# Performance work log

Measured on AMD Instinct MI355X. Metric: run time of the kernel, lower is better.

The kernel has to match this reference:

```python
import jax, jax.numpy as jnp
import numpy as np

NUM_HEADS = 8
FOCUSING_FACTOR = 3.0
EPS = 1e-6


def setup_inputs() -> dict:
    key = jax.random.key(0)
    ks = jax.random.split(key, 5)
    B, C, H, W = 16, 256, 64, 64
    hd = C // NUM_HEADS
    return {
        "x": jax.random.normal(ks[0], (B, C, H, W), jnp.float32),
        "qkv_w": jax.random.normal(ks[1], (3 * C, C), jnp.float32) * 0.02,
        "qkv_b": jnp.zeros((3 * C,), jnp.float32),
        "proj_w": jax.random.normal(ks[2], (C, C), jnp.float32) * 0.02,
        "proj_b": jnp.zeros((C,), jnp.float32),
        "dwc_w": jax.random.normal(ks[3], (hd, 1, 5, 5), jnp.float32) * 0.02,
        "dwc_b": jnp.zeros((hd,), jnp.float32),
        "scale": jnp.zeros((1, 1, C), jnp.float32),
    }


def reference(x, qkv_w, qkv_b, proj_w, proj_b, dwc_w, dwc_b, scale):
    B, C, H, W = x.shape
    N = H * W
    hd = C // NUM_HEADS

    # b c h w -> b (h w) c
    xf = x.reshape(B, C, N).transpose(0, 2, 1)
    qkv = xf @ qkv_w.T + qkv_b  # [B, N, 3C]
    q, k, v = jnp.split(qkv, 3, axis=-1)

    # focusing feature map
    q = jax.nn.relu(q) + EPS
    k = jax.nn.relu(k) + EPS
    sc = jax.nn.softplus(scale)
    q = q / sc
    k = k / sc
    q_norm = jnp.linalg.norm(q, axis=-1, keepdims=True)
    k_norm = jnp.linalg.norm(k, axis=-1, keepdims=True)
    # focusing_factor <= 6 branch
    q = q ** FOCUSING_FACTOR
    k = k ** FOCUSING_FACTOR
    q = q / jnp.linalg.norm(q, axis=-1, keepdims=True) * q_norm
    k = k / jnp.linalg.norm(k, axis=-1, keepdims=True) * k_norm

    # b n (h c) -> (b h) n c
    def to_heads(t):
        return t.reshape(B, N, NUM_HEADS, hd).transpose(0, 2, 1, 3).reshape(B * NUM_HEADS, N, hd)

    q, k, v = to_heads(q), to_heads(k), to_heads(v)

    i, j, c, d = N, N, hd, hd
    z = 1.0 / (jnp.einsum('bic,bc->bi', q, k.sum(axis=1)) + EPS)
    if i * j * (c + d) > c * d * (i + j):
        kv = jnp.einsum('bjc,bjd->bcd', k, v)  # [(BH), c, d]
        out = jnp.einsum('bic,bcd,bi->bid', q, kv, z)
    else:
        qk = jnp.einsum('bic,bjc->bij', q, k)
        out = jnp.einsum('bij,bjd,bi->bid', qk, v, z)

    # depthwise conv on v: b (w h) c -> b c w h (square map)
    num = int(N ** 0.5)
    fm = v.transpose(0, 2, 1).reshape(B * NUM_HEADS, hd, num, num)
    fm = jax.lax.conv_general_dilated(
        fm, dwc_w, window_strides=(1, 1), padding='SAME',
        feature_group_count=hd,
        dimension_numbers=('NCHW', 'OIHW', 'NCHW')) + dwc_b[None, :, None, None]
    fm = fm.reshape(B * NUM_HEADS, hd, N).transpose(0, 2, 1)
    out = out + fm

    # (b h) n c -> b n (h c)
    out = out.reshape(B, NUM_HEADS, N, hd).transpose(0, 2, 1, 3).reshape(B, N, C)
    out = out @ proj_w.T + proj_b
    # b (h w) c -> b c h w
    return out.transpose(0, 2, 1).reshape(B, C, H, W)
```

## Files before the change

### kernel.cpp

```cpp
#include <hip/hip_runtime.h>
#include <cmath>

#define B_   16
#define C_   256
#define HW_  64
#define N_   4096
#define NH_  8
#define HD_  32
#define M_   (B_ * N_)
#define QKVC (3 * C_)
#define EPS_ 1e-6f

typedef short bf16x8 __attribute__((ext_vector_type(8)));
typedef float f32x4 __attribute__((ext_vector_type(4)));
typedef unsigned int u32x4 __attribute__((ext_vector_type(4)));

__device__ __forceinline__ float b2f(unsigned short u) {
  union { unsigned int i; float f; } v;
  v.i = ((unsigned int)u) << 16;
  return v.f;
}
__device__ __forceinline__ float blo(unsigned int u) {
  union { unsigned int i; float f; } v; v.i = u << 16; return v.f;
}
__device__ __forceinline__ float bhi(unsigned int u) {
  union { unsigned int i; float f; } v; v.i = u & 0xffff0000u; return v.f;
}
__device__ __forceinline__ unsigned short f2b(float f) {
  union { float f; unsigned int i; } v;
  v.f = f;
  unsigned int r = v.i + 0x7FFFu + ((v.i >> 16) & 1u);
  return (unsigned short)(r >> 16);
}
__device__ __forceinline__ void gload_lds16(const void* g, void* l) {
  __builtin_amdgcn_global_load_lds(
      (const __attribute__((address_space(1))) void*)g,
      (__attribute__((address_space(3))) void*)l, 16, 0, 0);
}

__global__ __launch_bounds__(256) void k_cast_x(const float* __restrict__ x,
                                                unsigned short* __restrict__ xT) {
  __shared__ float t[32][33];
  const int n0 = blockIdx.x * 32, c0 = blockIdx.y * 32, b = blockIdx.z;
  const int tid = threadIdx.x;
  const int r = tid >> 3, g = (tid & 7) * 4;
  float4 v = *reinterpret_cast<const float4*>(
      &x[((size_t)(b * C_ + c0 + r)) * N_ + n0 + g]);
  t[r][g + 0] = v.x; t[r][g + 1] = v.y; t[r][g + 2] = v.z; t[r][g + 3] = v.w;
  __syncthreads();
  ushort4 o;
  o.x = f2b(t[g + 0][r]); o.y = f2b(t[g + 1][r]);
  o.z = f2b(t[g + 2][r]); o.w = f2b(t[g + 3][r]);
  *reinterpret_cast<ushort4*>(&xT[((size_t)(b * N_ + n0 + r)) * C_ + c0 + g]) = o;
}

__global__ __launch_bounds__(256) void k_cast_w(const float* __restrict__ w1,
                                                const float* __restrict__ w2,
                                                unsigned short* __restrict__ dst) {
  const int g4 = (blockIdx.x * 256 + threadIdx.x) * 4;
  float4 v;
  if (g4 < 196608) v = *reinterpret_cast<const float4*>(w1 + g4);
  else             v = *reinterpret_cast<const float4*>(w2 + (g4 - 196608));
  ushort4 o;
  o.x = f2b(v.x); o.y = f2b(v.y); o.z = f2b(v.z); o.w = f2b(v.w);
  *reinterpret_cast<ushort4*>(dst + g4) = o;
}

__global__ void k_prep_scale(const float* __restrict__ scale,
                             float* __restrict__ rsc) {
  const int c = threadIdx.x;
  rsc[c] = 1.f / log1pf(expf(scale[c]));
}

template <int LDA, int OUTMODE, int NCOL>
__global__ __launch_bounds__(256) void k_gemm(
    const unsigned short* __restrict__ A, const unsigned short* __restrict__ W,
    const float* __restrict__ bias, void* __restrict__ outp) {
  __shared__ unsigned short As[128 * 64];
  __shared__ unsigned short Bs[128 * 64];
  const int tid = threadIdx.x;
  const int wid = tid >> 6, lane = tid & 63;
  const int lin = blockIdx.x + blockIdx.y * 512;
  const int bandp = lin >> 3;
  const int rowb = bandp / NCOL;
  const int colb = bandp - rowb * NCOL;
  const int m0 = (((lin & 7) << 6) + rowb) * 128;
  const int col0 = colb * 128;
  const int wr = wid >> 1, wc = wid & 1;

  const int lrow = lane >> 3;
  const int sl = (lane & 7) ^ (lrow & 7);

  f32x4 acc[4][4];
#pragma unroll
  for (int i = 0; i < 4; ++i)
#pragma unroll
    for (int j = 0; j < 4; ++j) acc[i][j] = (f32x4){0.f, 0.f, 0.f, 0.f};

  for (int kt = 0; kt < 4; ++kt) {
    const int k0 = kt * 64;
#pragma unroll
    for (int q = 0; q < 4; ++q) {
      const int chunk = wid * 4 + q;
      const int row = chunk * 8 + lrow;
      gload_lds16(A + (size_t)(m0 + row) * LDA + k0 + sl * 8, &As[chunk * 512]);
      gload_lds16(W + (size_t)(col0 + row) * 256 + k0 + sl * 8, &Bs[chunk * 512]);
    }
    __syncthreads();

    bf16x8 fa[2][4], fb[2][4];
#pragma unroll
    for (int i = 0; i < 4; ++i) {
      const int ra = wr * 64 + i * 16 + (lane & 15);
      const int rb = wc * 64 + i * 16 + (lane & 15);
#pragma unroll
      for (int ks = 0; ks < 2; ++ks) {
        const int s = ks * 4 + (lane >> 4);
        fa[ks][i] = *reinterpret_cast<const bf16x8*>(
            &As[ra * 64 + ((s ^ (ra & 7)) * 8)]);
        fb[ks][i] = *reinterpret_cast<const bf16x8*>(
            &Bs[rb * 64 + ((s ^ (rb & 7)) * 8)]);
      }
    }
#pragma unroll
    for (int i = 0; i < 4; ++i)
#pragma unroll
      for (int j = 0; j < 4; ++j) {
        acc[i][j] = __builtin_amdgcn_mfma_f32_16x16x32_bf16(fa[0][i], fb[0][j],
                                                            acc[i][j], 0, 0, 0);
        acc[i][j] = __builtin_amdgcn_mfma_f32_16x16x32_bf16(fa[1][i], fb[1][j],
                                                            acc[i][j], 0, 0, 0);
      }
    __syncthreads();
  }

  if (OUTMODE == 0) {
    unsigned short* O = (unsigned short*)outp;
#pragma unroll
    for (int j = 0; j < 4; ++j) {
      const int colg = col0 + wc * 64 + j * 16 + (lane & 15);
      const float bb = bias[colg];
#pragma unroll
      for (int i = 0; i < 4; ++i) {
        const int mrow = m0 + wr * 64 + i * 16 + ((lane >> 4) << 2);
#pragma unroll
        for (int r = 0; r < 4; ++r)
          O[(size_t)(mrow + r) * QKVC + colg] = f2b(acc[i][j][r] + bb);
      }
    }
  } else {
    float* O = (float*)outp;
    const int b = m0 >> 12;
    const int nb0 = (m0 & 4095) + wr * 64;
#pragma unroll
    for (int j = 0; j < 4; ++j) {
      const int colg = col0 + wc * 64 + j * 16 + (lane & 15);
      const float bb = bias[colg];
#pragma unroll
      for (int i = 0; i < 4; ++i) {
        const int nb = nb0 + i * 16 + ((lane >> 4) << 2);
        f32x4 o = acc[i][j];
        o += bb;
        __builtin_nontemporal_store(
            o, reinterpret_cast<f32x4*>(&O[((size_t)(b * C_ + colg)) * N_ + nb]));
      }
    }
  }
}

__global__ __launch_bounds__(256) void k_focus(unsigned short* __restrict__ qkv,
                                               const float* __restrict__ rsc) {
  const int wave = threadIdx.x >> 6, lane = threadIdx.x & 63;
  const int t = blockIdx.x * 4 + wave;
  const size_t base = (size_t)t * QKVC + lane * 4;

  uint2 qu = *reinterpret_cast<const uint2*>(qkv + base);
  uint2 ku = *reinterpret_cast<const uint2*>(qkv + base + C_);
  const f32x4 rs = *reinterpret_cast<const f32x4*>(rsc + lane * 4);

  float q[4], k[4], q3[4], k3[4];
  q[0] = blo(qu.x); q[1] = bhi(qu.x); q[2] = blo(qu.y); q[3] = bhi(qu.y);
  k[0] = blo(ku.x); k[1] = bhi(ku.x); k[2] = blo(ku.y); k[3] = bhi(ku.y);

  float sq2 = 0.f, sq6 = 0.f, sk2 = 0.f, sk6 = 0.f;
#pragma unroll
  for (int i = 0; i < 4; ++i) {
    q[i] = (fmaxf(q[i], 0.f) + EPS_) * rs[i];
    k[i] = (fmaxf(k[i], 0.f) + EPS_) * rs[i];
    const float q2 = q[i] * q[i], k2 = k[i] * k[i];
    q3[i] = q2 * q[i];
    k3[i] = k2 * k[i];
    sq2 += q2; sk2 += k2;
    sq6 += q3[i] * q3[i];
    sk6 += k3[i] * k3[i];
  }
#pragma unroll
  for (int off = 1; off < 64; off <<= 1) {
    sq2 += __shfl_xor(sq2, off);
    sq6 += __shfl_xor(sq6, off);
    sk2 += __shfl_xor(sk2, off);
    sk6 += __shfl_xor(sk6, off);
  }
  const float fq = sqrtf(sq2 / sq6);
  const float fk = sqrtf(sk2 / sk6);

  uint2 oq, ok;
  oq.x = (unsigned int)f2b(q3[0] * fq) | ((unsigned int)f2b(q3[1] * fq) << 16);
  oq.y = (unsigned int)f2b(q3[2] * fq) | ((unsigned int)f2b(q3[3] * fq) << 16);
  ok.x = (unsigned int)f2b(k3[0] * fk) | ((unsigned int)f2b(k3[1] * fk) << 16);
  ok.y = (unsigned int)f2b(k3[2] * fk) | ((unsigned int)f2b(k3[3] * fk) << 16);
  *reinterpret_cast<uint2*>(qkv + base) = oq;
  *reinterpret_cast<uint2*>(qkv + base + C_) = ok;
}

#define KVP_CHUNKS 16
__global__ __launch_bounds__(256) void k_kv_part(
    const unsigned short* __restrict__ qkv, float* __restrict__ kvp,
    float* __restrict__ ksp) {
  const int bh = blockIdx.x;
  const int chunk = blockIdx.y;
  const int b = bh >> 3, h = bh & 7;
  const int tid = threadIdx.x;
  __shared__ float ksf[64 * 36];
  __shared__ float vsf[64 * 36];

  const int c = tid >> 3;
  const int d0 = (tid & 7) * 4;
  const int srow = tid >> 2;
  const int sseg = (tid & 3) * 8;
  const int j0 = chunk * 256;

  float a0 = 0.f, a1 = 0.f, a2 = 0.f, a3 = 0.f, ksum = 0.f;

  uint4 ku, vu;
  {
    const size_t rb = ((size_t)(b * N_ + j0 + srow)) * QKVC + h * HD_ + sseg;
    ku = *reinterpret_cast<const uint4*>(qkv + rb + C_);
    vu = *reinterpret_cast<const uint4*>(qkv + rb + 2 * C_);
  }

  for (int t = 0; t < 4; ++t) {
    {
      f32x4 k0 = {blo(ku.x), bhi(ku.x), blo(ku.y), bhi(ku.y)};
      f32x4 k1 = {blo(ku.z), bhi(ku.z), blo(ku.w), bhi(ku.w)};
      f32x4 v0 = {blo(vu.x), bhi(vu.x), blo(vu.y), bhi(vu.y)};
      f32x4 v1 = {blo(vu.z), bhi(vu.z), blo(vu.w), bhi(vu.w)};
      *reinterpret_cast<f32x4*>(&ksf[srow * 36 + sseg]) = k0;
      *reinterpret_cast<f32x4*>(&ksf[srow * 36 + sseg + 4]) = k1;
      *reinterpret_cast<f32x4*>(&vsf[srow * 36 + sseg]) = v0;
      *reinterpret_cast<f32x4*>(&vsf[srow * 36 + sseg + 4]) = v1;
    }
    __syncthreads();
    if (t < 3) {
      const size_t rb =
          ((size_t)(b * N_ + j0 + (t + 1) * 64 + srow)) * QKVC + h * HD_ + sseg;
      ku = *reinterpret_cast<const uint4*>(qkv + rb + C_);
      vu = *reinterpret_cast<const uint4*>(qkv + rb + 2 * C_);
    }
#pragma unroll 8
    for (int jj = 0; jj < 64; ++jj) {
      const float kc = ksf[jj * 36 + c];
      const f32x4 vv = *reinterpret_cast<const f32x4*>(&vsf[jj * 36 + d0]);
      a0 += kc * vv[0];
      a1 += kc * vv[1];
      a2 += kc * vv[2];
      a3 += kc * vv[3];
      ksum += kc;
    }
    __syncthreads();
  }

  float* kvo = kvp + ((size_t)chunk * 128 + bh) * 1024 + c * 32 + d0;
  kvo[0] = a0; kvo[1] = a1; kvo[2] = a2; kvo[3] = a3;
  if ((tid & 7) == 0) ksp[((size_t)chunk * 128 + bh) * 32 + c] = ksum;
}

__global__ __launch_bounds__(256) void k_attn_mfma(
    unsigned short* __restrict__ qkv, const float* __restrict__ kvp,
    const float* __restrict__ ksp) {
  const int bh = blockIdx.y;
  const int b = bh >> 3, h = bh & 7;
  const int tid = threadIdx.x;
  const int lane = tid & 63;
  const int r0 = blockIdx.x * 256 + (tid >> 6) * 64;

  __shared__ float kv_s[1024];
  __shared__ float ksum_s[32];
  for (int pp = tid; pp < 1024; pp += 256) {
    float s = 0.f;
#pragma unroll
    for (int ch = 0; ch < KVP_CHUNKS; ++ch)
      s += kvp[((size_t)ch * 128 + bh) * 1024 + pp];
    kv_s[pp] = s;
  }
  if (tid < 32) {
    float s = 0.f;
#pragma unroll
    for (int ch = 0; ch < KVP_CHUNKS; ++ch)
      s += ksp[((size_t)ch * 128 + bh) * 32 + tid];
    ksum_s[tid] = s;
  }
  __syncthreads();

  const int kb = (lane >> 4) * 8;
  const int col = lane & 15;
  bf16x8 bhi0, bhi1, blo0, blo1;
  float ks0[8];
#pragma unroll
  for (int t = 0; t < 8; ++t) {
    const float v0 = kv_s[(kb + t) * 32 + col];
    const float v1 = kv_s[(kb + t) * 32 + col + 16];
    const unsigned short h0 = f2b(v0), h1 = f2b(v1);
    ((unsigned short*)&bhi0)[t] = h0;
    ((unsigned short*)&bhi1)[t] = h1;
    ((unsigned short*)&blo0)[t] = f2b(v0 - b2f(h0));
    ((unsigned short*)&blo1)[t] = f2b(v1 - b2f(h1));
    ks0[t] = ksum_s[kb + t];
  }

#pragma unroll
  for (int rt = 0; rt < 4; ++rt) {
    const int row = r0 + rt * 16 + (lane & 15);
    const bf16x8 a = *reinterpret_cast<const bf16x8*>(
        qkv + (size_t)(b * N_ + row) * QKVC + h * HD_ + kb);
    float zp = 0.f;
#pragma unroll
    for (int t = 0; t < 8; ++t) zp += b2f(((const unsigned short*)&a)[t]) * ks0[t];
    zp += __shfl_xor(zp, 16);
    zp += __shfl_xor(zp, 32);
    const float z = 1.f / (zp + EPS_);

    f32x4 acc0 = {0.f, 0.f, 0.f, 0.f}, acc1 = {0.f, 0.f, 0.f, 0.f};
    acc0 = __builtin_amdgcn_mfma_f32_16x16x32_bf16(a, blo0, acc0, 0, 0, 0);
    acc1 = __builtin_amdgcn_mfma_f32_16x16x32_bf16(a, blo1, acc1, 0, 0, 0);
    acc0 = __builtin_amdgcn_mfma_f32_16x16x32_bf16(a, bhi0, acc0, 0, 0, 0);
    acc1 = __builtin_amdgcn_mfma_f32_16x16x32_bf16(a, bhi1, acc1, 0, 0, 0);

#pragma unroll
    for (int r = 0; r < 4; ++r) {
      const int rr = (lane >> 4) * 4 + r;
      const float zr = __shfl(z, rr);
      unsigned short* op =
          qkv + (size_t)(b * N_ + r0 + rt * 16 + rr) * QKVC + h * HD_;
      op[col] = f2b(acc0[r] * zr);
      op[col + 16] = f2b(acc1[r] * zr);
    }
  }
}

__global__ __launch_bounds__(256) void k_conv(
    unsigned short* __restrict__ qkv, const float* __restrict__ dwc_w,
    const float* __restrict__ dwc_b) {
  const int lin = blockIdx.x;
  const int g2 = (lin & 7) * 256 + (lin >> 3);
  const int bh = g2 >> 4;
  const int ig = g2 & 15;
  const int i0 = ig * 4;
  const int b = bh >> 3, h = bh & 7;
  const int tid = threadIdx.x;
  const int j = tid >> 2;
  const int g = tid & 3;
  const int d0 = g * 8;
  const int wave = tid >> 6, lane = tid & 63;

  __shared__ float w_s[800];
  __shared__ float b_s[32];
  __shared__ unsigned short v_s[8 * 64 * 32];

#pragma unroll
  for (int rr = 0; rr < 8; ++rr) {
    const int ii = i0 + rr - 2;
    if (ii < 0 || ii >= 64) continue;
    gload_lds16(qkv + ((size_t)(b * N_ + ii * 64 + wave * 16 + (lane >> 2))) * QKVC +
                    2 * C_ + h * HD_ + (lane & 3) * 8,
                &v_s[rr * 2048 + wave * 512]);
  }
  for (int p = tid; p < 800; p += 256)
    w_s[p] = dwc_w[(p & 31) * 25 + (p >> 5)];
  if (tid < 32) b_s[tid] = dwc_b[tid];
  __syncthreads();

#pragma unroll
  for (int r = 0; r < 4; ++r) {
    const int i = i0 + r;
    float fm[8];
#pragma unroll
    for (int dd = 0; dd < 8; ++dd) fm[dd] = b_s[d0 + dd];
#pragma unroll
    for (int kr = 0; kr < 5; ++kr) {
      const int ii = i + kr - 2;
      if (ii < 0 || ii >= 64) continue;
      const int lr = r + kr;
#pragma unroll
      for (int kj = 0; kj < 5; ++kj) {
        const int jj = j + kj - 2;
        if (jj < 0 || jj >= 64) continue;
        const unsigned int* vr = reinterpret_cast<const unsigned int*>(
            &v_s[lr * 2048 + jj * 32 + d0]);
        const float* wt = &w_s[(kr * 5 + kj) * 32 + d0];
#pragma unroll
        for (int p = 0; p < 4; ++p) {
          const unsigned int vu = vr[p];
          fm[2 * p + 0] += blo(vu) * wt[2 * p + 0];
          fm[2 * p + 1] += bhi(vu) * wt[2 * p + 1];
        }
      }
    }
    unsigned int* orow = reinterpret_cast<unsigned int*>(
        qkv + ((size_t)(b * N_ + i * 64 + j)) * QKVC + h * HD_ + d0);
    uint4 cur = *reinterpret_cast<const uint4*>(orow);
    unsigned int o[4] = {cur.x, cur.y, cur.z, cur.w};
#pragma unroll
    for (int p = 0; p < 4; ++p) {
      const unsigned int lo = f2b(blo(o[p]) + fm[2 * p + 0]);
      const unsigned int hi = f2b(bhi(o[p]) + fm[2 * p + 1]);
      o[p] = lo | (hi << 16);
    }
    *reinterpret_cast<uint4*>(orow) = make_uint4(o[0], o[1], o[2], o[3]);
  }
}

extern "C" void kernel_launch(void* const* d_in, const int* in_sizes, int n_in,
                              void* d_out, int out_size, void* d_ws,
                              size_t ws_size, hipStream_t stream) {
  (void)in_sizes; (void)n_in; (void)out_size; (void)ws_size;
  const float* x      = (const float*)d_in[0];
  const float* qkv_w  = (const float*)d_in[1];
  const float* qkv_b  = (const float*)d_in[2];
  const float* proj_w = (const float*)d_in[3];
  const float* proj_b = (const float*)d_in[4];
  const float* dwc_w  = (const float*)d_in[5];
  const float* dwc_b  = (const float*)d_in[6];
  const float* scale  = (const float*)d_in[7];
  float* out = (float*)d_out;

  char* w = (char*)d_ws;
  unsigned short* xT   = (unsigned short*)w; w += (size_t)M_ * C_ * 2;
  unsigned short* qkvb = (unsigned short*)w; w += (size_t)M_ * QKVC * 2;
  unsigned short* wq   = (unsigned short*)w; w += (size_t)(QKVC + C_) * C_ * 2;
  unsigned short* wp   = wq + (size_t)QKVC * C_;
  float* kvp   = (float*)w;                  w += (size_t)KVP_CHUNKS * 128 * 1024 * 4;
  float* ksp   = (float*)w;                  w += (size_t)KVP_CHUNKS * 128 * 32 * 4;
  float* rscb  = (float*)w;                  w += 256 * 4;

  k_prep_scale<<<1, 256, 0, stream>>>(scale, rscb);
  k_cast_x<<<dim3(N_ / 32, C_ / 32, B_), 256, 0, stream>>>(x, xT);
  k_cast_w<<<256, 256, 0, stream>>>(qkv_w, proj_w, wq);
  k_gemm<256, 0, 6><<<dim3(512, 6), 256, 0, stream>>>(
      xT, wq, qkv_b, (void*)qkvb);
  k_focus<<<M_ / 4, 256, 0, stream>>>(qkvb, rscb);
  k_kv_part<<<dim3(128, KVP_CHUNKS), 256, 0, stream>>>(qkvb, kvp, ksp);
  k_attn_mfma<<<dim3(N_ / 256, 128), 256, 0, stream>>>(qkvb, kvp, ksp);
  k_conv<<<2048, 256, 0, stream>>>(qkvb, dwc_w, dwc_b);
  k_gemm<768, 1, 2><<<dim3(512, 2), 256, 0, stream>>>(
      qkvb, wp, proj_b, (void*)out);
}
```

Baseline: 210.7 us.

## Fuse attention output and depthwise conv into one kernel; drop nontemporal stores

Measured after the change: 202.8 us. -3.8%, faster.

```diff
diff --git a/kernel.cpp b/kernel.cpp
--- a/kernel.cpp
+++ b/kernel.cpp
@@ -161,8 +161,7 @@
         const int nb = nb0 + i * 16 + ((lane >> 4) << 2);
         f32x4 o = acc[i][j];
         o += bb;
-        __builtin_nontemporal_store(
-            o, reinterpret_cast<f32x4*>(&O[((size_t)(b * C_ + colg)) * N_ + nb]));
+        *reinterpret_cast<f32x4*>(&O[((size_t)(b * C_ + colg)) * N_ + nb]) = o;
       }
     }
   }
@@ -275,81 +274,9 @@
   if ((tid & 7) == 0) ksp[((size_t)chunk * 128 + bh) * 32 + c] = ksum;
 }
 
-__global__ __launch_bounds__(256) void k_attn_mfma(
+__global__ __launch_bounds__(256) void k_attn_conv_f(
     unsigned short* __restrict__ qkv, const float* __restrict__ kvp,
-    const float* __restrict__ ksp) {
-  const int bh = blockIdx.y;
-  const int b = bh >> 3, h = bh & 7;
-  const int tid = threadIdx.x;
-  const int lane = tid & 63;
-  const int r0 = blockIdx.x * 256 + (tid >> 6) * 64;
-
-  __shared__ float kv_s[1024];
-  __shared__ float ksum_s[32];
-  for (int pp = tid; pp < 1024; pp += 256) {
-    float s = 0.f;
-#pragma unroll
-    for (int ch = 0; ch < KVP_CHUNKS; ++ch)
-      s += kvp[((size_t)ch * 128 + bh) * 1024 + pp];
-    kv_s[pp] = s;
-  }
-  if (tid < 32) {
-    float s = 0.f;
-#pragma unroll
-    for (int ch = 0; ch < KVP_CHUNKS; ++ch)
-      s += ksp[((size_t)ch * 128 + bh) * 32 + tid];
-    ksum_s[tid] = s;
-  }
-  __syncthreads();
-
-  const int kb = (lane >> 4) * 8;
-  const int col = lane & 15;
-  bf16x8 bhi0, bhi1, blo0, blo1;
-  float ks0[8];
-#pragma unroll
-  for (int t = 0; t < 8; ++t) {
-    const float v0 = kv_s[(kb + t) * 32 + col];
-    const float v1 = kv_s[(kb + t) * 32 + col + 16];
-    const unsigned short h0 = f2b(v0), h1 = f2b(v1);
-    ((unsigned short*)&bhi0)[t] = h0;
-    ((unsigned short*)&bhi1)[t] = h1;
-    ((unsigned short*)&blo0)[t] = f2b(v0 - b2f(h0));
-    ((unsigned short*)&blo1)[t] = f2b(v1 - b2f(h1));
-    ks0[t] = ksum_s[kb + t];
-  }
-
-#pragma unroll
-  for (int rt = 0; rt < 4; ++rt) {
-    const int row = r0 + rt * 16 + (lane & 15);
-    const bf16x8 a = *reinterpret_cast<const bf16x8*>(
-        qkv + (size_t)(b * N_ + row) * QKVC + h * HD_ + kb);
-    float zp = 0.f;
-#pragma unroll
-    for (int t = 0; t < 8; ++t) zp += b2f(((const unsigned short*)&a)[t]) * ks0[t];
-    zp += __shfl_xor(zp, 16);
-    zp += __shfl_xor(zp, 32);
-    const float z = 1.f / (zp + EPS_);
-
-    f32x4 acc0 = {0.f, 0.f, 0.f, 0.f}, acc1 = {0.f, 0.f, 0.f, 0.f};
-    acc0 = __builtin_amdgcn_mfma_f32_16x16x32_bf16(a, blo0, acc0, 0, 0, 0);
-    acc1 = __builtin_amdgcn_mfma_f32_16x16x32_bf16(a, blo1, acc1, 0, 0, 0);
-    acc0 = __builtin_amdgcn_mfma_f32_16x16x32_bf16(a, bhi0, acc0, 0, 0, 0);
-    acc1 = __builtin_amdgcn_mfma_f32_16x16x32_bf16(a, bhi1, acc1, 0, 0, 0);
-
-#pragma unroll
-    for (int r = 0; r < 4; ++r) {
-      const int rr = (lane >> 4) * 4 + r;
-      const float zr = __shfl(z, rr);
-      unsigned short* op =
-          qkv + (size_t)(b * N_ + r0 + rt * 16 + rr) * QKVC + h * HD_;
-      op[col] = f2b(acc0[r] * zr);
-      op[col + 16] = f2b(acc1[r] * zr);
-    }
-  }
-}
-
-__global__ __launch_bounds__(256) void k_conv(
-    unsigned short* __restrict__ qkv, const float* __restrict__ dwc_w,
+    const float* __restrict__ ksp, const float* __restrict__ dwc_w,
     const float* __restrict__ dwc_b) {
   const int lin = blockIdx.x;
   const int g2 = (lin & 7) * 256 + (lin >> 3);
@@ -358,14 +285,32 @@
   const int i0 = ig * 4;
   const int b = bh >> 3, h = bh & 7;
   const int tid = threadIdx.x;
-  const int j = tid >> 2;
-  const int g = tid & 3;
-  const int d0 = g * 8;
   const int wave = tid >> 6, lane = tid & 63;
 
+  __shared__ float kv_s[1024];
+  __shared__ float ksum_s[32];
   __shared__ float w_s[800];
   __shared__ float b_s[32];
   __shared__ unsigned short v_s[8 * 64 * 32];
+
+  for (int pp = tid; pp < 1024; pp += 256) {
+    float s = 0.f;
+#pragma unroll
+    for (int ch = 0; ch < KVP_CHUNKS; ++ch)
+      s += kvp[((size_t)ch * 128 + bh) * 1024 + pp];
+    kv_s[pp] = s;
+  }
+  if (tid < 32) {
+    float s = 0.f;
+#pragma unroll
+    for (int ch = 0; ch < KVP_CHUNKS; ++ch)
+      s += ksp[((size_t)ch * 128 + bh) * 32 + tid];
+    ksum_s[tid] = s;
+  }
+  for (int p = tid; p < 800; p += 256)
+    w_s[p] = dwc_w[(p & 31) * 25 + (p >> 5)];
+  if (tid < 32) b_s[tid] = dwc_b[tid];
+  __syncthreads();
 
 #pragma unroll
   for (int rr = 0; rr < 8; ++rr) {
@@ -375,48 +320,97 @@
                     2 * C_ + h * HD_ + (lane & 3) * 8,
                 &v_s[rr * 2048 + wave * 512]);
   }
-  for (int p = tid; p < 800; p += 256)
-    w_s[p] = dwc_w[(p & 31) * 25 + (p >> 5)];
-  if (tid < 32) b_s[tid] = dwc_b[tid];
+
+  {
+    const int kb = (lane >> 4) * 8;
+    const int col = lane & 15;
+    bf16x8 bh0, bh1, bl0, bl1;
+    float ks0[8];
+#pragma unroll
+    for (int t = 0; t < 8; ++t) {
+      const float v0 = kv_s[(kb + t) * 32 + col];
+      const float v1 = kv_s[(kb + t) * 32 + col + 16];
+      const unsigned short h0 = f2b(v0), h1 = f2b(v1);
+      ((unsigned short*)&bh0)[t] = h0;
+      ((unsigned short*)&bh1)[t] = h1;
+      ((unsigned short*)&bl0)[t] = f2b(v0 - b2f(h0));
+      ((unsigned short*)&bl1)[t] = f2b(v1 - b2f(h1));
+      ks0[t] = ksum_s[kb + t];
+    }
+    const int r0 = (i0 + wave) * 64;
+#pragma unroll
+    for (int rt = 0; rt < 4; ++rt) {
+      const int row = r0 + rt * 16 + (lane & 15);
+      const bf16x8 a = *reinterpret_cast<const bf16x8*>(
+          qkv + (size_t)(b * N_ + row) * QKVC + h * HD_ + kb);
+      float zp = 0.f;
+#pragma unroll
+      for (int t = 0; t < 8; ++t)
+        zp += b2f(((const unsigned short*)&a)[t]) * ks0[t];
+      zp += __shfl_xor(zp, 16);
+      zp += __shfl_xor(zp, 32);
+      const float z = 1.f / (zp + EPS_);
+
+      f32x4 acc0 = {0.f, 0.f, 0.f, 0.f}, acc1 = {0.f, 0.f, 0.f, 0.f};
+      acc0 = __builtin_amdgcn_mfma_f32_16x16x32_bf16(a, bl0, acc0, 0, 0, 0);
+      acc1 = __builtin_amdgcn_mfma_f32_16x16x32_bf16(a, bl1, acc1, 0, 0, 0);
+      acc0 = __builtin_amdgcn_mfma_f32_16x16x32_bf16(a, bh0, acc0, 0, 0, 0);
+      acc1 = __builtin_amdgcn_mfma_f32_16x16x32_bf16(a, bh1, acc1, 0, 0, 0);
+
+#pragma unroll
+      for (int r = 0; r < 4; ++r) {
+        const int rr = (lane >> 4) * 4 + r;
+        const float zr = __shfl(z, rr);
+        unsigned short* op =
+            qkv + (size_t)(b * N_ + r0 + rt * 16 + rr) * QKVC + h * HD_;
+        op[col] = f2b(acc0[r] * zr);
+        op[col + 16] = f2b(acc1[r] * zr);
+      }
+    }
+  }
   __syncthreads();
 
-#pragma unroll
-  for (int r = 0; r < 4; ++r) {
-    const int i = i0 + r;
-    float fm[8];
-#pragma unroll
-    for (int dd = 0; dd < 8; ++dd) fm[dd] = b_s[d0 + dd];
-#pragma unroll
-    for (int kr = 0; kr < 5; ++kr) {
-      const int ii = i + kr - 2;
-      if (ii < 0 || ii >= 64) continue;
-      const int lr = r + kr;
-#pragma unroll
-      for (int kj = 0; kj < 5; ++kj) {
-        const int jj = j + kj - 2;
-        if (jj < 0 || jj >= 64) continue;
-        const unsigned int* vr = reinterpret_cast<const unsigned int*>(
-            &v_s[lr * 2048 + jj * 32 + d0]);
-        const float* wt = &w_s[(kr * 5 + kj) * 32 + d0];
-#pragma unroll
-        for (int p = 0; p < 4; ++p) {
-          const unsigned int vu = vr[p];
-          fm[2 * p + 0] += blo(vu) * wt[2 * p + 0];
-          fm[2 * p + 1] += bhi(vu) * wt[2 * p + 1];
+  {
+    const int j = tid >> 2;
+    const int d0 = (tid & 3) * 8;
+#pragma unroll
+    for (int r = 0; r < 4; ++r) {
+      const int i = i0 + r;
+      float fm[8];
+#pragma unroll
+      for (int dd = 0; dd < 8; ++dd) fm[dd] = b_s[d0 + dd];
+#pragma unroll
+      for (int kr = 0; kr < 5; ++kr) {
+        const int ii = i + kr - 2;
+        if (ii < 0 || ii >= 64) continue;
+        const int lr = r + kr;
+#pragma unroll
+        for (int kj = 0; kj < 5; ++kj) {
+          const int jj = j + kj - 2;
+          if (jj < 0 || jj >= 64) continue;
+          const unsigned int* vr = reinterpret_cast<const unsigned int*>(
+              &v_s[lr * 2048 + jj * 32 + d0]);
+          const float* wt = &w_s[(kr * 5 + kj) * 32 + d0];
+#pragma unroll
+          for (int p = 0; p < 4; ++p) {
+            const unsigned int vu = vr[p];
+            fm[2 * p + 0] += blo(vu) * wt[2 * p + 0];
+            fm[2 * p + 1] += bhi(vu) * wt[2 * p + 1];
+          }
         }
       }
-    }
-    unsigned int* orow = reinterpret_cast<unsigned int*>(
-        qkv + ((size_t)(b * N_ + i * 64 + j)) * QKVC + h * HD_ + d0);
-    uint4 cur = *reinterpret_cast<const uint4*>(orow);
-    unsigned int o[4] = {cur.x, cur.y, cur.z, cur.w};
-#pragma unroll
-    for (int p = 0; p < 4; ++p) {
-      const unsigned int lo = f2b(blo(o[p]) + fm[2 * p + 0]);
-      const unsigned int hi = f2b(bhi(o[p]) + fm[2 * p + 1]);
-      o[p] = lo | (hi << 16);
-    }
-    *reinterpret_cast<uint4*>(orow) = make_uint4(o[0], o[1], o[2], o[3]);
+      unsigned int* orow = reinterpret_cast<unsigned int*>(
+          qkv + ((size_t)(b * N_ + i * 64 + j)) * QKVC + h * HD_ + d0);
+      uint4 cur = *reinterpret_cast<const uint4*>(orow);
+      unsigned int o[4] = {cur.x, cur.y, cur.z, cur.w};
+#pragma unroll
+      for (int p = 0; p < 4; ++p) {
+        const unsigned int lo = f2b(blo(o[p]) + fm[2 * p + 0]);
+        const unsigned int hi = f2b(bhi(o[p]) + fm[2 * p + 1]);
+        o[p] = lo | (hi << 16);
+      }
+      *reinterpret_cast<uint4*>(orow) = make_uint4(o[0], o[1], o[2], o[3]);
+    }
   }
 }
 
@@ -450,8 +444,7 @@
       xT, wq, qkv_b, (void*)qkvb);
   k_focus<<<M_ / 4, 256, 0, stream>>>(qkvb, rscb);
   k_kv_part<<<dim3(128, KVP_CHUNKS), 256, 0, stream>>>(qkvb, kvp, ksp);
-  k_attn_mfma<<<dim3(N_ / 256, 128), 256, 0, stream>>>(qkvb, kvp, ksp);
-  k_conv<<<2048, 256, 0, stream>>>(qkvb, dwc_w, dwc_b);
+  k_attn_conv_f<<<2048, 256, 0, stream>>>(qkvb, kvp, ksp, dwc_w, dwc_b);
   k_gemm<768, 1, 2><<<dim3(512, 2), 256, 0, stream>>>(
       qkvb, wp, proj_b, (void*)out);
 }
```
